# Optimization experiments

Measured on AMD Instinct MI355X. Metric: run time of the kernel, lower is better.

Reference implementation:

```python
import jax, jax.numpy as jnp
import numpy as np

B, S, D, N = 8, 4096, 768, 64


def setup_inputs() -> dict:
    key = jax.random.key(0)
    k1, k2 = jax.random.split(key)
    word_vectors = jax.random.normal(k1, (B, S, D), dtype=jnp.float32)
    sent_rep_token_ids = jnp.sort(jax.random.randint(k2, (B, N), 0, S), axis=1)
    sent_rep_mask = jnp.ones((B, N), dtype=jnp.float32)
    # sent_lengths: each row must sum exactly to S (torch.split contract).
    rng = np.random.default_rng(0)
    lens = np.stack([
        np.diff(np.concatenate([[0], np.sort(rng.choice(np.arange(1, S), N - 1, replace=False)), [S]]))
        for _ in range(B)
    ])
    sent_lengths = jnp.asarray(lens, dtype=jnp.int64) if jax.config.jax_enable_x64 else jnp.asarray(lens, dtype=jnp.int32)
    sent_lengths_mask = jnp.ones((B, N), dtype=jnp.float32)
    return {
        "word_vectors": word_vectors,
        "sent_rep_token_ids": sent_rep_token_ids,
        "sent_rep_mask": sent_rep_mask,
        "sent_lengths": sent_lengths,
        "sent_lengths_mask": sent_lengths_mask,
    }


def reference(word_vectors, sent_rep_token_ids, sent_rep_mask, sent_lengths, sent_lengths_mask):
    b, s, d = word_vectors.shape
    n = sent_lengths.shape[1]
    dt = word_vectors.dtype

    # --- sent_rep_tokens branch: gather CLS-style token per sentence ---
    rep_vec = jnp.take_along_axis(word_vectors, sent_rep_token_ids[:, :, None], axis=1)  # [B,N,D]
    rep_vec = rep_vec * sent_rep_mask[:, :, None].astype(dt)

    # --- mean_tokens branch: ragged per-segment mean via segment_sum ---
    ends = jnp.cumsum(sent_lengths, axis=1)                      # [B,N] exclusive-end offsets
    pos = jnp.arange(s)
    seg = jax.vmap(lambda e: jnp.searchsorted(e, pos, side='right'))(ends)  # [B,S] segment id per token
    gseg = (seg + jnp.arange(b)[:, None] * n).reshape(-1)        # global segment ids [B*S]
    flat = word_vectors.reshape(b * s, d)
    sums = jax.ops.segment_sum(flat, gseg, num_segments=b * n).reshape(b, n, d)
    counts = jax.ops.segment_sum((flat != 0).astype(dt), gseg, num_segments=b * n).reshape(b, n, d)
    mean = sums / jnp.maximum(counts, 1)
    # fallback to word_vectors[0,0] when a segment has zero nonzero entries (original semantics)
    all_zero = (counts.sum(axis=-1) == 0)                        # [B,N]
    mean = jnp.where(all_zero[:, :, None], word_vectors[0, 0], mean)
    mean_vec = mean * sent_lengths_mask[:, :, None].astype(dt)

    out_vectors = jnp.concatenate([rep_vec, mean_vec], axis=1)   # [B,2N,D]
    out_masks = jnp.concatenate([sent_rep_mask, sent_lengths_mask], axis=1)  # [B,2N]
    return out_vectors, out_masks
```

## Files before the change

### kernel.cpp

```cpp
#include <hip/hip_runtime.h>

#define BB 8
#define SS 4096
#define DD 768
#define NN 64
#define D4 (DD / 4)
#define CHT 128
#define MAXCH 96
#define NREC (BB * MAXCH)

typedef float nfloat4 __attribute__((ext_vector_type(4)));

__global__ __launch_bounds__(256) void chunk_kernel(
    const float* __restrict__ wv,
    const int* __restrict__ lens,
    float* __restrict__ ws_sum,
    unsigned char* __restrict__ ws_cnt)
{
    const int cidx = blockIdx.x;
    const int b    = blockIdx.y;
    const int g    = blockIdx.z;
    const int tid  = threadIdx.x;
    const int lane = tid & 63;
    const int w    = tid >> 6;

    const int l    = lens[b * NN + lane];
    const int nchl = (l + CHT - 1) >> 7;
    int inclen = l, inch = nchl;
    #pragma unroll
    for (int off = 1; off < 64; off <<= 1) {
        int a = __shfl_up(inclen, off); if (lane >= off) inclen += a;
        int c = __shfl_up(inch,   off); if (lane >= off) inch   += c;
    }
    const int total_ch = __shfl(inch, 63);
    if (cidx >= total_ch) return;

    unsigned long long m = __ballot(inch > cidx);
    const int n         = __ffsll(m) - 1;
    const int seg_len   = __shfl(l, n);
    const int seg_start = __shfl(inclen, n) - seg_len;
    const int ch_base   = __shfl(inch, n) - __shfl(nchl, n);
    const int t0 = seg_start + (cidx - ch_base) * CHT;
    const int t1 = min(seg_start + seg_len, t0 + CHT);

    const int col4 = g * 64 + lane;
    const nfloat4* base = (const nfloat4*)wv + (size_t)b * SS * D4 + col4;

    float4 s = make_float4(0.f, 0.f, 0.f, 0.f);
    float4 c = make_float4(0.f, 0.f, 0.f, 0.f);
    #pragma unroll 8
    for (int t = t0 + w; t < t1; t += 4) {
        nfloat4 v = __builtin_nontemporal_load(base + (size_t)t * D4);
        s.x += v.x; s.y += v.y; s.z += v.z; s.w += v.w;
        c.x += (v.x != 0.f) ? 1.f : 0.f;
        c.y += (v.y != 0.f) ? 1.f : 0.f;
        c.z += (v.z != 0.f) ? 1.f : 0.f;
        c.w += (v.w != 0.f) ? 1.f : 0.f;
    }

    __shared__ float4 s_s[4][64];
    __shared__ float4 s_c[4][64];
    s_s[w][lane] = s;
    s_c[w][lane] = c;
    __syncthreads();

    if (tid < 64) {
        float4 S = make_float4(0.f, 0.f, 0.f, 0.f);
        float4 C = make_float4(0.f, 0.f, 0.f, 0.f);
        #pragma unroll
        for (int j = 0; j < 4; ++j) {
            float4 a = s_s[j][tid], d = s_c[j][tid];
            S.x += a.x; S.y += a.y; S.z += a.z; S.w += a.w;
            C.x += d.x; C.y += d.y; C.z += d.z; C.w += d.w;
        }
        const size_t rec = (size_t)(b * MAXCH + cidx);
        ((float4*)ws_sum)[rec * D4 + g * 64 + tid] = S;
        uchar4 u;
        u.x = (unsigned char)C.x; u.y = (unsigned char)C.y;
        u.z = (unsigned char)C.z; u.w = (unsigned char)C.w;
        ((uchar4*)ws_cnt)[rec * D4 + g * 64 + tid] = u;
    }
}

__global__ __launch_bounds__(256) void finalize_kernel(
    const float* __restrict__ wv,
    const int* __restrict__ rep_ids,
    const float* __restrict__ rep_mask,
    const int* __restrict__ lens,
    const float* __restrict__ len_mask,
    const float* __restrict__ ws_sum,
    const unsigned char* __restrict__ ws_cnt,
    float* __restrict__ out)
{
    __shared__ float s_part[4];
    __shared__ int s_info[2];
    const int sgid = blockIdx.x;
    const int b = sgid >> 6, n = sgid & 63;
    const int tid = threadIdx.x;
    const int lane = tid & 63;

    if (tid < 64) {
        const int l    = lens[b * NN + tid];
        const int nchl = (l + CHT - 1) >> 7;
        int inch = nchl;
        #pragma unroll
        for (int off = 1; off < 64; off <<= 1) {
            int a = __shfl_up(inch, off); if (lane >= off) inch += a;
        }
        if (tid == n) { s_info[0] = inch - nchl; s_info[1] = nchl; }
    }
    __syncthreads();
    const int ch_base = s_info[0];
    const int K       = s_info[1];
    const bool active = tid < D4;

    float4 S = make_float4(0,0,0,0), C = S;
    if (active) {
        for (int k = 0; k < K; ++k) {
            const size_t rec = (size_t)(b * MAXCH + ch_base + k);
            float4 sv = ((const float4*)ws_sum)[rec * D4 + tid];
            uchar4 cv = ((const uchar4*)ws_cnt)[rec * D4 + tid];
            S.x += sv.x; S.y += sv.y; S.z += sv.z; S.w += sv.w;
            C.x += (float)cv.x; C.y += (float)cv.y;
            C.z += (float)cv.z; C.w += (float)cv.w;
        }
    }

    float tot = C.x + C.y + C.z + C.w;
    #pragma unroll
    for (int off = 32; off; off >>= 1) tot += __shfl_xor(tot, off);
    if ((tid & 63) == 0) s_part[tid >> 6] = tot;
    __syncthreads();
    const float total = s_part[0] + s_part[1] + s_part[2] + s_part[3];

    if (active) {
        float4 mean;
        mean.x = S.x / fmaxf(C.x, 1.f);
        mean.y = S.y / fmaxf(C.y, 1.f);
        mean.z = S.z / fmaxf(C.z, 1.f);
        mean.w = S.w / fmaxf(C.w, 1.f);
        if (total == 0.f) mean = ((const float4*)wv)[tid];

        const float lm = len_mask[sgid];
        mean.x *= lm; mean.y *= lm; mean.z *= lm; mean.w *= lm;

        float4* out4 = (float4*)out;
        out4[(size_t)(b * 2 * NN + NN + n) * D4 + tid] = mean;

        const int   rid = rep_ids[sgid];
        const float rm  = rep_mask[sgid];
        float4 rv = ((const float4*)wv)[(size_t)(b * SS + rid) * D4 + tid];
        rv.x *= rm; rv.y *= rm; rv.z *= rm; rv.w *= rm;
        out4[(size_t)(b * 2 * NN + n) * D4 + tid] = rv;

        if (tid == 0) {
            float* masks = out + (size_t)BB * 2 * NN * DD;
            masks[b * 2 * NN + n]      = rm;
            masks[b * 2 * NN + NN + n] = lm;
        }
    }
}

extern "C" void kernel_launch(void* const* d_in, const int* in_sizes, int n_in,
                              void* d_out, int out_size, void* d_ws, size_t ws_size,
                              hipStream_t stream) {
    const float* wv       = (const float*)d_in[0];
    const int*   rep_ids  = (const int*)d_in[1];
    const float* rep_mask = (const float*)d_in[2];
    const int*   lens     = (const int*)d_in[3];
    const float* len_mask = (const float*)d_in[4];
    float*       out      = (float*)d_out;
    float*         ws_sum = (float*)d_ws;
    unsigned char* ws_cnt = (unsigned char*)d_ws + (size_t)NREC * DD * 4;

    dim3 gridB(MAXCH, BB, 3);
    chunk_kernel<<<gridB, 256, 0, stream>>>(wv, lens, ws_sum, ws_cnt);
    finalize_kernel<<<BB * NN, 256, 0, stream>>>(wv, rep_ids, rep_mask, lens,
                                                 len_mask, ws_sum, ws_cnt, out);
}
```

Measured before the change: 157.0 us.

## Replace per-segment chunk partials with fixed token windows and atomic accumulation

Result: slower. 176.8 us (+12.6%).

```diff
diff --git a/kernel.cpp b/kernel.cpp
--- a/kernel.cpp
+++ b/kernel.cpp
@@ -5,125 +5,107 @@
 #define DD 768
 #define NN 64
 #define D4 (DD / 4)
-#define CHT 128
-#define MAXCH 96
-#define NREC (BB * MAXCH)
+#define NWIN 32
+#define WTOK 128
+#define ACC_FLOATS (BB * NN * DD)
 
 typedef float nfloat4 __attribute__((ext_vector_type(4)));
 
-__global__ __launch_bounds__(256) void chunk_kernel(
+__global__ __launch_bounds__(256) void zero_kernel(float4* __restrict__ ws) {
+    const size_t i = (size_t)blockIdx.x * 256 + threadIdx.x;
+    ws[i] = make_float4(0.f, 0.f, 0.f, 0.f);
+}
+
+__global__ __launch_bounds__(256) void window_kernel(
     const float* __restrict__ wv,
     const int* __restrict__ lens,
-    float* __restrict__ ws_sum,
-    unsigned char* __restrict__ ws_cnt)
+    float* __restrict__ gsum,
+    float* __restrict__ gcnt)
 {
-    const int cidx = blockIdx.x;
+    const int win  = blockIdx.x;
     const int b    = blockIdx.y;
     const int g    = blockIdx.z;
     const int tid  = threadIdx.x;
     const int lane = tid & 63;
     const int w    = tid >> 6;
 
-    const int l    = lens[b * NN + lane];
-    const int nchl = (l + CHT - 1) >> 7;
-    int inclen = l, inch = nchl;
+    int e = lens[b * NN + lane];
     #pragma unroll
     for (int off = 1; off < 64; off <<= 1) {
-        int a = __shfl_up(inclen, off); if (lane >= off) inclen += a;
-        int c = __shfl_up(inch,   off); if (lane >= off) inch   += c;
+        int a = __shfl_up(e, off); if (lane >= off) e += a;
     }
-    const int total_ch = __shfl(inch, 63);
-    if (cidx >= total_ch) return;
 
-    unsigned long long m = __ballot(inch > cidx);
-    const int n         = __ffsll(m) - 1;
-    const int seg_len   = __shfl(l, n);
-    const int seg_start = __shfl(inclen, n) - seg_len;
-    const int ch_base   = __shfl(inch, n) - __shfl(nchl, n);
-    const int t0 = seg_start + (cidx - ch_base) * CHT;
-    const int t1 = min(seg_start + seg_len, t0 + CHT);
+    const int tstart = win * WTOK + w * 32;
+    const int tend   = tstart + 32;
+    const int col4   = g * 64 + lane;
+    const nfloat4* base = (const nfloat4*)wv + (size_t)b * SS * D4 + col4;
 
-    const int col4 = g * 64 + lane;
-    const nfloat4* base = (const nfloat4*)wv + (size_t)b * SS * D4 + col4;
+    int seg     = __popcll(__ballot(e <= tstart));
+    int cur_end = __shfl(e, seg);
 
     float4 s = make_float4(0.f, 0.f, 0.f, 0.f);
     float4 c = make_float4(0.f, 0.f, 0.f, 0.f);
-    #pragma unroll 8
-    for (int t = t0 + w; t < t1; t += 4) {
-        nfloat4 v = __builtin_nontemporal_load(base + (size_t)t * D4);
-        s.x += v.x; s.y += v.y; s.z += v.z; s.w += v.w;
-        c.x += (v.x != 0.f) ? 1.f : 0.f;
-        c.y += (v.y != 0.f) ? 1.f : 0.f;
-        c.z += (v.z != 0.f) ? 1.f : 0.f;
-        c.w += (v.w != 0.f) ? 1.f : 0.f;
+
+    #define ACC(T)                                                      \
+        {                                                               \
+            nfloat4 v = __builtin_nontemporal_load(base + (size_t)(T) * D4); \
+            s.x += v.x; s.y += v.y; s.z += v.z; s.w += v.w;             \
+            c.x += (v.x != 0.f) ? 1.f : 0.f;                            \
+            c.y += (v.y != 0.f) ? 1.f : 0.f;                            \
+            c.z += (v.z != 0.f) ? 1.f : 0.f;                            \
+            c.w += (v.w != 0.f) ? 1.f : 0.f;                            \
+        }
+
+    #define FLUSH(SG)                                                   \
+        {                                                               \
+            float* ps = gsum + ((size_t)(b * NN + (SG)) * D4 + col4) * 4; \
+            float* pc = gcnt + ((size_t)(b * NN + (SG)) * D4 + col4) * 4; \
+            atomicAdd(ps + 0, s.x); atomicAdd(ps + 1, s.y);             \
+            atomicAdd(ps + 2, s.z); atomicAdd(ps + 3, s.w);             \
+            atomicAdd(pc + 0, c.x); atomicAdd(pc + 1, c.y);             \
+            atomicAdd(pc + 2, c.z); atomicAdd(pc + 3, c.w);             \
+        }
+
+    if (cur_end >= tend) {
+        #pragma unroll 8
+        for (int t = tstart; t < tend; ++t) ACC(t);
+        FLUSH(seg);
+    } else {
+        for (int t = tstart; t < tend; ++t) {
+            if (t >= cur_end) {
+                FLUSH(seg);
+                s = make_float4(0.f, 0.f, 0.f, 0.f);
+                c = make_float4(0.f, 0.f, 0.f, 0.f);
+                seg     = __popcll(__ballot(e <= t));
+                cur_end = __shfl(e, seg);
+            }
+            ACC(t);
+        }
+        FLUSH(seg);
     }
-
-    __shared__ float4 s_s[4][64];
-    __shared__ float4 s_c[4][64];
-    s_s[w][lane] = s;
-    s_c[w][lane] = c;
-    __syncthreads();
-
-    if (tid < 64) {
-        float4 S = make_float4(0.f, 0.f, 0.f, 0.f);
-        float4 C = make_float4(0.f, 0.f, 0.f, 0.f);
-        #pragma unroll
-        for (int j = 0; j < 4; ++j) {
-            float4 a = s_s[j][tid], d = s_c[j][tid];
-            S.x += a.x; S.y += a.y; S.z += a.z; S.w += a.w;
-            C.x += d.x; C.y += d.y; C.z += d.z; C.w += d.w;
-        }
-        const size_t rec = (size_t)(b * MAXCH + cidx);
-        ((float4*)ws_sum)[rec * D4 + g * 64 + tid] = S;
-        uchar4 u;
-        u.x = (unsigned char)C.x; u.y = (unsigned char)C.y;
-        u.z = (unsigned char)C.z; u.w = (unsigned char)C.w;
-        ((uchar4*)ws_cnt)[rec * D4 + g * 64 + tid] = u;
-    }
+    #undef ACC
+    #undef FLUSH
 }
 
 __global__ __launch_bounds__(256) void finalize_kernel(
     const float* __restrict__ wv,
     const int* __restrict__ rep_ids,
     const float* __restrict__ rep_mask,
-    const int* __restrict__ lens,
     const float* __restrict__ len_mask,
-    const float* __restrict__ ws_sum,
-    const unsigned char* __restrict__ ws_cnt,
+    const float* __restrict__ gsum,
+    const float* __restrict__ gcnt,
     float* __restrict__ out)
 {
     __shared__ float s_part[4];
-    __shared__ int s_info[2];
     const int sgid = blockIdx.x;
     const int b = sgid >> 6, n = sgid & 63;
     const int tid = threadIdx.x;
-    const int lane = tid & 63;
-
-    if (tid < 64) {
-        const int l    = lens[b * NN + tid];
-        const int nchl = (l + CHT - 1) >> 7;
-        int inch = nchl;
-        #pragma unroll
-        for (int off = 1; off < 64; off <<= 1) {
-            int a = __shfl_up(inch, off); if (lane >= off) inch += a;
-        }
-        if (tid == n) { s_info[0] = inch - nchl; s_info[1] = nchl; }
-    }
-    __syncthreads();
-    const int ch_base = s_info[0];
-    const int K       = s_info[1];
     const bool active = tid < D4;
 
     float4 S = make_float4(0,0,0,0), C = S;
     if (active) {
-        for (int k = 0; k < K; ++k) {
-            const size_t rec = (size_t)(b * MAXCH + ch_base + k);
-            float4 sv = ((const float4*)ws_sum)[rec * D4 + tid];
-            uchar4 cv = ((const uchar4*)ws_cnt)[rec * D4 + tid];
-            S.x += sv.x; S.y += sv.y; S.z += sv.z; S.w += sv.w;
-            C.x += (float)cv.x; C.y += (float)cv.y;
-            C.z += (float)cv.z; C.w += (float)cv.w;
-        }
+        S = ((const float4*)gsum)[(size_t)sgid * D4 + tid];
+        C = ((const float4*)gcnt)[(size_t)sgid * D4 + tid];
     }
 
     float tot = C.x + C.y + C.z + C.w;
@@ -170,11 +152,11 @@
     const int*   lens     = (const int*)d_in[3];
     const float* len_mask = (const float*)d_in[4];
     float*       out      = (float*)d_out;
-    float*         ws_sum = (float*)d_ws;
-    unsigned char* ws_cnt = (unsigned char*)d_ws + (size_t)NREC * DD * 4;
+    float* gsum = (float*)d_ws;
+    float* gcnt = (float*)d_ws + ACC_FLOATS;
 
-    dim3 gridB(MAXCH, BB, 3);
-    chunk_kernel<<<gridB, 256, 0, stream>>>(wv, lens, ws_sum, ws_cnt);
-    finalize_kernel<<<BB * NN, 256, 0, stream>>>(wv, rep_ids, rep_mask, lens,
-                                                 len_mask, ws_sum, ws_cnt, out);
+    zero_kernel<<<768, 256, 0, stream>>>((float4*)d_ws);
+    window_kernel<<<dim3(NWIN, BB, 3), 256, 0, stream>>>(wv, lens, gsum, gcnt);
+    finalize_kernel<<<BB * NN, 256, 0, stream>>>(wv, rep_ids, rep_mask,
+                                                 len_mask, gsum, gcnt, out);
 }
```
